# Optimization experiments

Hardware: AMD Instinct MI355X
Metric: run time of the kernel (lower is better)

## Reference

```python
import jax, jax.numpy as jnp
import numpy as np

B, H, W, DIM = 2, 128, 128, 256
HEADS, DHEAD = 16, 64
INNER = HEADS * DHEAD  # 1024
EPS = 1e-5  # BatchNorm eps


def _dwconv(x, w, groups):
    # x: [b, c_in, h, w], w: [c_out, c_in//groups, 3, 3], pad=1, stride=1
    return jax.lax.conv_general_dilated(
        x, w, window_strides=(1, 1), padding=((1, 1), (1, 1)),
        dimension_numbers=('NCHW', 'OIHW', 'NCHW'), feature_group_count=groups)


def _bn(x, gamma, beta, mean, var):
    # inference-mode BatchNorm2d over channel dim of NCHW
    inv = gamma * jax.lax.rsqrt(var + EPS)
    return (x - mean[None, :, None, None]) * inv[None, :, None, None] + beta[None, :, None, None]


def setup_inputs() -> dict:
    key = jax.random.key(0)
    ks = jax.random.split(key, 12)
    d = {}
    d['x_in'] = jax.random.normal(ks[0], (B, H, W, DIM), jnp.float32)
    def convw(k, cout):
        return jax.random.normal(k, (cout, 1, 3, 3), jnp.float32) * 0.1
    d['wq'] = convw(ks[1], INNER)
    d['wk'] = convw(ks[2], INNER)
    d['wv'] = convw(ks[3], INNER)
    for name, k in zip(('q', 'k', 'v'), (ks[4], ks[5], ks[6])):
        k0, k1 = jax.random.split(k)
        d[f'bn{name}_g'] = 1.0 + 0.1 * jax.random.normal(k0, (INNER,), jnp.float32)
        d[f'bn{name}_b'] = 0.05 * jax.random.normal(k1, (INNER,), jnp.float32)
        d[f'bn{name}_m'] = jnp.zeros((INNER,), jnp.float32)
        d[f'bn{name}_v'] = jnp.ones((INNER,), jnp.float32)
    d['rescale'] = jnp.ones((HEADS, 1, 1), jnp.float32)
    d['proj_w'] = jax.random.normal(ks[7], (DIM, INNER), jnp.float32) / np.sqrt(INNER).astype(np.float32)
    d['proj_b'] = jnp.zeros((DIM,), jnp.float32)
    d['pos_w1'] = convw(ks[8], DIM)
    d['pos_w2'] = convw(ks[9], DIM)
    return d


def _forward(x_in, wq, wk, wv,
             bnq_g, bnq_b, bnq_m, bnq_v,
             bnk_g, bnk_b, bnk_m, bnk_v,
             bnv_g, bnv_b, bnv_m, bnv_v,
             rescale, proj_w, proj_b, pos_w1, pos_w2):
    b, h, w, c = x_in.shape
    n = h * w
    x = jnp.transpose(x_in, (0, 3, 1, 2))  # [b, c, h, w]

    def proj_path(wc, g, be, m, va):
        y = _bn(_dwconv(x, wc, c), g, be, m, va)        # [b, INNER, h, w]
        return y.reshape(b, INNER, n).transpose(0, 2, 1)  # 'b c h w -> b (h w) c'

    q_inp = proj_path(wq, bnq_g, bnq_b, bnq_m, bnq_v)  # [b, n, INNER]
    k_inp = proj_path(wk, bnk_g, bnk_b, bnk_m, bnk_v)
    v_inp = proj_path(wv, bnv_g, bnv_b, bnv_m, bnv_v)

    def to_heads(t):
        # 'b n (h d) -> b h n d' then transpose(-2,-1) -> [b, heads, d, n]
        return t.reshape(b, n, HEADS, DHEAD).transpose(0, 2, 3, 1)

    q = to_heads(q_inp)
    k = to_heads(k_inp)
    v = to_heads(v_inp)
    # L2 normalize along token dim (last axis), torch F.normalize eps=1e-12
    q = q / jnp.clip(jnp.linalg.norm(q, axis=-1, keepdims=True), 1e-12)
    k = k / jnp.clip(jnp.linalg.norm(k, axis=-1, keepdims=True), 1e-12)

    attn = jnp.einsum('bhdn,bhen->bhde', k, q) * rescale[None]  # [b, heads, d, d]
    attn = jax.nn.softmax(attn, axis=-1)
    xo = jnp.einsum('bhde,bhen->bhdn', attn, v)  # [b, heads, d, n]
    # faithful to torch: raw reshape of [b, heads, d, n] -> [b, n, heads*d]
    xo = xo.reshape(b, n, HEADS * DHEAD)

    out_c = (xo @ proj_w.T + proj_b).reshape(b, h, w, c)

    vp = (v_inp @ proj_w.T + proj_b).reshape(b, h, w, c).transpose(0, 3, 1, 2)
    pe = _dwconv(jax.nn.gelu(_dwconv(vp, pos_w1, c), approximate=False), pos_w2, c)
    out_p = pe.transpose(0, 2, 3, 1)
    return out_c + out_p


def reference(x_in, wq, wk, wv,
              bnq_g, bnq_b, bnq_m, bnq_v,
              bnk_g, bnk_b, bnk_m, bnk_v,
              bnv_g, bnv_b, bnv_m, bnv_v,
              rescale, proj_w, proj_b, pos_w1, pos_w2):
    return _forward(x_in, wq, wk, wv,
                    bnq_g, bnq_b, bnq_m, bnq_v,
                    bnk_g, bnk_b, bnk_m, bnk_v,
                    bnv_g, bnv_b, bnv_m, bnv_v,
                    rescale, proj_w, proj_b, pos_w1, pos_w2)
```

## Files before the change

kernel.cpp:

```cpp
#include <hip/hip_runtime.h>

#define NTOK 16384
#define CDIM 256
#define INNER 1024
#define WW 128
#define HH 128

typedef unsigned short bf16_t;
typedef __bf16 bf16x8 __attribute__((ext_vector_type(8)));
typedef float f32x4 __attribute__((ext_vector_type(4)));

__device__ __forceinline__ float bf2f(bf16_t u) {
    union { unsigned int i; float f; } x;
    x.i = ((unsigned int)u) << 16;
    return x.f;
}
__device__ __forceinline__ bf16_t f2bf(float f) {
    union { float f; unsigned int i; } x;
    x.f = f;
    unsigned int r = x.i + 0x7FFFu + ((x.i >> 16) & 1u);
    return (bf16_t)(r >> 16);
}
__device__ __forceinline__ unsigned int cvtpk(float a, float b) {
    unsigned int r;
    asm("v_cvt_pk_bf16_f32 %0, %1, %2" : "=v"(r) : "v"(a), "v"(b));
    return r;
}

static const size_t OFF_VT   = 16777216;
static const size_t OFF_XO   = 83886080;
static const size_t OFF_VP   = 150994944;
static const size_t OFF_PE2  = 184549376;
static const size_t OFF_WBF  = 201326592;
static const size_t OFF_S    = 218103808;
static const size_t OFF_SSQ  = 218628096;
static const size_t OFF_SSK  = 218636288;

__global__ __launch_bounds__(512, 4) void k12_fused(
    const float* __restrict__ x,
    const float* __restrict__ wq, const float* __restrict__ wk, const float* __restrict__ wv,
    const float* __restrict__ qg, const float* __restrict__ qb, const float* __restrict__ qm, const float* __restrict__ qv,
    const float* __restrict__ kg, const float* __restrict__ kb, const float* __restrict__ km, const float* __restrict__ kv_,
    const float* __restrict__ vg, const float* __restrict__ vb, const float* __restrict__ vm, const float* __restrict__ vv,
    bf16_t* __restrict__ vt, float* __restrict__ S,
    float* __restrict__ ssq, float* __restrict__ ssk) {
    int chunk = blockIdx.x;
    int h = blockIdx.y;
    int b = blockIdx.z;
    int y0 = chunk * 8;

    __shared__ ushort taps[16][10][132];
    __shared__ ushort Qs[64][72];
    __shared__ ushort Ks[64][72];
    __shared__ unsigned int Vs32[64][34];

    int tid = threadIdx.x;
    int lane = tid & 63, wave = tid >> 6;

    {
        const float* xb = x + (size_t)b * NTOK * CDIM + h * 16;
        for (int u = tid; u < 5200; u += 512) {
            int pos = u >> 2, quad = u & 3;
            int i = pos / 130, c = pos - i * 130;
            int gy = y0 - 1 + i, gx = c - 1;
            if (gy >= 0 && gy < HH && gx >= 0 && gx < WW) {
                float4 v = *(const float4*)&xb[(size_t)(gy * WW + gx) * CDIM + quad * 4];
                taps[quad * 4 + 0][i][c] = f2bf(v.x);
                taps[quad * 4 + 1][i][c] = f2bf(v.y);
                taps[quad * 4 + 2][i][c] = f2bf(v.z);
                taps[quad * 4 + 3][i][c] = f2bf(v.w);
            } else {
                taps[quad * 4 + 0][i][c] = 0;
                taps[quad * 4 + 1][i][c] = 0;
                taps[quad * 4 + 2][i][c] = 0;
                taps[quad * 4 + 3][i][c] = 0;
            }
        }
    }

    int tq = tid & 15;
    int pc = (tid >> 4) & 15;
    int ts = tid >> 8;

    const float* wsrc = ts ? wk : wq;
    const float* gp = ts ? kg : qg;
    const float* bp = ts ? kb : qb;
    const float* mp = ts ? km : qm;
    const float* vp_ = ts ? kv_ : qv;
    int chbase = h * 64 + pc * 4;
    float wQK[4][9], shQK[4];
#pragma unroll
    for (int s = 0; s < 4; s++) {
        int ch = chbase + s;
        float sc = gp[ch] * rsqrtf(vp_[ch] + 1e-5f);
        shQK[s] = bp[ch] - mp[ch] * sc;
#pragma unroll
        for (int t = 0; t < 9; t++) wQK[s][t] = wsrc[(size_t)ch * 9 + t] * sc;
    }
    float wV[2][9], shV[2];
#pragma unroll
    for (int sv = 0; sv < 2; sv++) {
        int ch = chbase + 2 * ts + sv;
        float sc = vg[ch] * rsqrtf(vv[ch] + 1e-5f);
        shV[sv] = vb[ch] - vm[ch] * sc;
#pragma unroll
        for (int t = 0; t < 9; t++) wV[sv][t] = wv[(size_t)ch * 9 + t] * sc;
    }

    ushort (*QK)[72] = ts ? Ks : Qs;

    int wm = wave & 1;
    int wn4 = wave >> 1;
    int qd = lane >> 4, l16 = lane & 15;
    f32x4 acc[2];
    acc[0] = (f32x4){0.f, 0.f, 0.f, 0.f};
    acc[1] = (f32x4){0.f, 0.f, 0.f, 0.f};

    int vrow = tid >> 3;
    int vseg = tid & 7;
    bf16_t* vtb = vt + (size_t)b * 16777216 + (size_t)h * 64;

    float ssl[4] = {0.f, 0.f, 0.f, 0.f};

    __syncthreads();

#pragma unroll 1
    for (int kc = 0; kc < 1024; kc += 64) {
        int grp = kc >> 6;
        int ly = grp >> 1;
        int xh = (grp & 1) << 6;
        int x0 = xh + tq * 4;

        float tp[3][6];
#pragma unroll
        for (int i = 0; i < 3; i++) {
            const ushort* rp = &taps[pc][ly + i][x0];
            ushort4 u4 = *(const ushort4*)rp;
            ushort2 u2 = *(const ushort2*)(rp + 4);
            tp[i][0] = bf2f(u4.x); tp[i][1] = bf2f(u4.y);
            tp[i][2] = bf2f(u4.z); tp[i][3] = bf2f(u4.w);
            tp[i][4] = bf2f(u2.x); tp[i][5] = bf2f(u2.y);
        }

#pragma unroll
        for (int s = 0; s < 4; s++) {
            float o0 = shQK[s], o1 = shQK[s], o2 = shQK[s], o3 = shQK[s];
#pragma unroll
            for (int i = 0; i < 3; i++) {
                float wa = wQK[s][i * 3 + 0], wb = wQK[s][i * 3 + 1], wc = wQK[s][i * 3 + 2];
                o0 += wa * tp[i][0] + wb * tp[i][1] + wc * tp[i][2];
                o1 += wa * tp[i][1] + wb * tp[i][2] + wc * tp[i][3];
                o2 += wa * tp[i][2] + wb * tp[i][3] + wc * tp[i][4];
                o3 += wa * tp[i][3] + wb * tp[i][4] + wc * tp[i][5];
            }
            ssl[s] += o0 * o0 + o1 * o1 + o2 * o2 + o3 * o3;
            uint2 pk;
            pk.x = cvtpk(o0, o1);
            pk.y = cvtpk(o2, o3);
            *(uint2*)&QK[pc * 4 + s][tq * 4] = pk;
        }

        {
            float ov[2][4];
#pragma unroll
            for (int sv = 0; sv < 2; sv++) {
                float o0 = shV[sv], o1 = shV[sv], o2 = shV[sv], o3 = shV[sv];
#pragma unroll
                for (int i = 0; i < 3; i++) {
                    float wa = wV[sv][i * 3 + 0], wb = wV[sv][i * 3 + 1], wc = wV[sv][i * 3 + 2];
                    o0 += wa * tp[i][0] + wb * tp[i][1] + wc * tp[i][2];
                    o1 += wa * tp[i][1] + wb * tp[i][2] + wc * tp[i][3];
                    o2 += wa * tp[i][2] + wb * tp[i][3] + wc * tp[i][4];
                    o3 += wa * tp[i][3] + wb * tp[i][4] + wc * tp[i][5];
                }
                ov[sv][0] = o0; ov[sv][1] = o1; ov[sv][2] = o2; ov[sv][3] = o3;
            }
#pragma unroll
            for (int j = 0; j < 4; j++)
                Vs32[tq * 4 + j][pc * 2 + ts] = cvtpk(ov[0][j], ov[1][j]);
        }

        __syncthreads();

        {
            uint4 o4;
            o4.x = Vs32[vrow][vseg * 4 + 0];
            o4.y = Vs32[vrow][vseg * 4 + 1];
            o4.z = Vs32[vrow][vseg * 4 + 2];
            o4.w = Vs32[vrow][vseg * 4 + 3];
            *(uint4*)&vtb[(size_t)(chunk * 1024 + kc + vrow) * 1024 + vseg * 8] = o4;
        }

#pragma unroll
        for (int kk = 0; kk < 64; kk += 32) {
            bf16x8 af0 = *(const bf16x8*)&Ks[wm * 32 + l16][kk + qd * 8];
            bf16x8 af1 = *(const bf16x8*)&Ks[wm * 32 + 16 + l16][kk + qd * 8];
            bf16x8 bf0 = *(const bf16x8*)&Qs[wn4 * 16 + l16][kk + qd * 8];
            acc[0] = __builtin_amdgcn_mfma_f32_16x16x32_bf16(af0, bf0, acc[0], 0, 0, 0);
            acc[1] = __builtin_amdgcn_mfma_f32_16x16x32_bf16(af1, bf0, acc[1], 0, 0, 0);
        }

        __syncthreads();
    }

    float* Sb = S + (size_t)(b * 16 + h) * 4096;
#pragma unroll
    for (int i = 0; i < 2; i++)
#pragma unroll
        for (int r = 0; r < 4; r++) {
            int d = wm * 32 + i * 16 + qd * 4 + r;
            int e = wn4 * 16 + l16;
            atomicAdd(&Sb[(size_t)d * 64 + e], acc[i][r]);
        }

#pragma unroll
    for (int s = 0; s < 4; s++) {
        float v = ssl[s];
#pragma unroll
        for (int o = 1; o < 16; o <<= 1) v += __shfl_xor(v, o, 64);
        ssl[s] = v;
    }
    if ((lane & 15) == 0) {
        float* dst = (ts ? ssk : ssq) + b * INNER + chbase;
        atomicAdd(&dst[0], ssl[0]);
        atomicAdd(&dst[1], ssl[1]);
        atomicAdd(&dst[2], ssl[2]);
        atomicAdd(&dst[3], ssl[3]);
    }
}

__global__ __launch_bounds__(64) void k3_softmax(float* __restrict__ S,
                                                 const float* __restrict__ ssq,
                                                 const float* __restrict__ ssk,
                                                 const float* __restrict__ rescale) {
    int bh = blockIdx.x;
    int b = bh >> 4, h = bh & 15;
    int d = threadIdx.x;
    __shared__ float rq[64];
    int cbase = b * INNER + h * 64;
    rq[d] = 1.0f / fmaxf(sqrtf(ssq[cbase + d]), 1e-12f);
    float rk = 1.0f / fmaxf(sqrtf(ssk[cbase + d]), 1e-12f);
    __syncthreads();
    float rsc = rescale[h];
    const float* row = S + (size_t)bh * 4096 + (size_t)d * 64;
    float sv[64];
    float mx = -3.4e38f;
#pragma unroll
    for (int e = 0; e < 64; e++) {
        sv[e] = row[e] * rk * rq[e] * rsc;
        mx = fmaxf(mx, sv[e]);
    }
    float sum = 0.f;
#pragma unroll
    for (int e = 0; e < 64; e++) {
        sv[e] = expf(sv[e] - mx);
        sum += sv[e];
    }
    float inv = 1.0f / sum;
    __syncthreads();
    ushort* attn = (ushort*)((char*)S + (size_t)bh * 16384);
#pragma unroll
    for (int e = 0; e < 64; e++) attn[d * 64 + e] = f2bf(sv[e] * inv);
}

__global__ __launch_bounds__(256) void cvt_w(const float* __restrict__ w,
                                             bf16_t* __restrict__ wbf) {
    int i = (blockIdx.x * 256 + threadIdx.x) * 4;
    float4 f = *(const float4*)&w[i];
    ushort4 r;
    r.x = f2bf(f.x); r.y = f2bf(f.y); r.z = f2bf(f.z); r.w = f2bf(f.w);
    *(ushort4*)&wbf[i] = r;
}

__global__ __launch_bounds__(256) void k4_mfma(const float* __restrict__ Sbase,
                                               const bf16_t* __restrict__ vt,
                                               bf16_t* __restrict__ xo) {
    int tt = blockIdx.x;
    int h = blockIdx.y;
    int b = blockIdx.z;
    int bh = b * 16 + h;
    const ushort* attn = (const ushort*)((const char*)Sbase + (size_t)bh * 16384);
    __shared__ ushort As[64][72];
    __shared__ ushort Bs[128][72];
    int tid = threadIdx.x, lane = tid & 63, wave = tid >> 6;
    int wm = wave & 1, wn = wave >> 1;
    int qd = lane >> 4, l16 = lane & 15;
    int r0 = tid >> 3, c0 = (tid & 7) * 8;
#pragma unroll
    for (int l = 0; l < 2; l++) {
        int row = r0 + l * 32;
        *(uint4*)&As[row][c0] = *(const uint4*)&attn[row * 64 + c0];
    }
    const bf16_t* vtb = vt + (size_t)b * 16777216 + (size_t)(tt * 128) * 1024 + h * 64;
#pragma unroll
    for (int l = 0; l < 4; l++) {
        int row = r0 + l * 32;
        *(uint4*)&Bs[row][c0] = *(const uint4*)&vtb[(size_t)row * 1024 + c0];
    }
    __syncthreads();
    f32x4 acc[2][4];
#pragma unroll
    for (int i = 0; i < 2; i++)
#pragma unroll
        for (int j = 0; j < 4; j++) acc[i][j] = (f32x4){0.f, 0.f, 0.f, 0.f};
#pragma unroll
    for (int kk = 0; kk < 64; kk += 32) {
        bf16x8 af[2], bfr[4];
#pragma unroll
        for (int i = 0; i < 2; i++)
            af[i] = *(const bf16x8*)&As[wm * 32 + i * 16 + l16][kk + qd * 8];
#pragma unroll
        for (int j = 0; j < 4; j++)
            bfr[j] = *(const bf16x8*)&Bs[wn * 64 + j * 16 + l16][kk + qd * 8];
#pragma unroll
        for (int i = 0; i < 2; i++)
#pragma unroll
            for (int j = 0; j < 4; j++)
                acc[i][j] = __builtin_amdgcn_mfma_f32_16x16x32_bf16(af[i], bfr[j], acc[i][j], 0, 0, 0);
    }
    bf16_t* xob = xo + (size_t)b * 16777216 + (size_t)(h * 64) * NTOK + (size_t)tt * 128;
#pragma unroll
    for (int i = 0; i < 2; i++)
#pragma unroll
        for (int j = 0; j < 4; j++)
#pragma unroll
            for (int r = 0; r < 4; r++) {
                int d = wm * 32 + i * 16 + qd * 4 + r;
                int t = wn * 64 + j * 16 + l16;
                xob[(size_t)d * NTOK + t] = f2bf(acc[i][j][r]);
            }
}

template <int FUSE_PE2>
__global__ __launch_bounds__(256) void gemm_tn(
    const bf16_t* __restrict__ A, const bf16_t* __restrict__ B,
    const float* __restrict__ pb, void* __restrict__ Cv,
    int lda, int ldb, int ldc, int K,
    long strideA, long strideB, long strideC, int bias_on_n,
    const bf16_t* __restrict__ pe2) {
    int mb = blockIdx.x, nb = blockIdx.y, b = blockIdx.z;
    A += (size_t)b * strideA;
    B += (size_t)b * strideB;
    __shared__ ushort smem[2 * 128 * 72];
    ushort (*As)[72] = (ushort(*)[72])smem;
    ushort (*Bs)[72] = (ushort(*)[72])(smem + 128 * 72);
    int tid = threadIdx.x;
    int lane = tid & 63, wave = tid >> 6;
    int wm = wave & 1, wn = wave >> 1;
    int q = lane >> 4, l16 = lane & 15;
    f32x4 acc[4][4];
#pragma unroll
    for (int i = 0; i < 4; i++)
#pragma unroll
        for (int j = 0; j < 4; j++) acc[i][j] = (f32x4){0.f, 0.f, 0.f, 0.f};
    const bf16_t* Ab = A + (size_t)mb * 128 * lda;
    const bf16_t* Bb = B + (size_t)nb * 128 * ldb;
    int r0 = tid >> 3;
    int c0 = (tid & 7) * 8;
#pragma unroll 1
    for (int kc = 0; kc < K; kc += 64) {
#pragma unroll
        for (int l = 0; l < 4; l++) {
            int row = l * 32 + r0;
            *(uint4*)&As[row][c0] = *(const uint4*)&Ab[(size_t)row * lda + kc + c0];
            *(uint4*)&Bs[row][c0] = *(const uint4*)&Bb[(size_t)row * ldb + kc + c0];
        }
        __syncthreads();
#pragma unroll
        for (int kk = 0; kk < 64; kk += 32) {
            bf16x8 af[4], bfr[4];
#pragma unroll
            for (int i = 0; i < 4; i++)
                af[i] = *(const bf16x8*)&As[wm * 64 + i * 16 + l16][kk + q * 8];
#pragma unroll
            for (int j = 0; j < 4; j++)
                bfr[j] = *(const bf16x8*)&Bs[wn * 64 + j * 16 + l16][kk + q * 8];
#pragma unroll
            for (int i = 0; i < 4; i++)
#pragma unroll
                for (int j = 0; j < 4; j++)
                    acc[i][j] = __builtin_amdgcn_mfma_f32_16x16x32_bf16(af[i], bfr[j], acc[i][j], 0, 0, 0);
        }
        __syncthreads();
    }
    if (FUSE_PE2) {
        const bf16_t* peb = pe2 + (size_t)b * 4194304;
        int gm0 = mb * 128, gn0 = nb * 128;
        for (int u = tid; u < 128 * 16; u += 256) {
            int row = u >> 4, seg = u & 15;
            *(uint4*)&smem[row * 132 + seg * 8] =
                *(const uint4*)&peb[(size_t)(gn0 + row) * NTOK + gm0 + seg * 8];
        }
        __syncthreads();
        float* C = (float*)Cv + (size_t)b * strideC;
#pragma unroll
        for (int i = 0; i < 4; i++) {
#pragma unroll
            for (int j = 0; j < 4; j++) {
                int n = wn * 64 + j * 16 + l16;
                int gn = gn0 + n;
                int m0 = wm * 64 + i * 16 + q * 4;
                ushort4 pv4 = *(const ushort4*)&smem[n * 132 + m0];
                float bias = pb[gn];
#pragma unroll
                for (int r = 0; r < 4; r++) {
                    ushort pu = (r == 0) ? pv4.x : ((r == 1) ? pv4.y : ((r == 2) ? pv4.z : pv4.w));
                    C[(size_t)(gm0 + m0 + r) * ldc + gn] = acc[i][j][r] + bias + bf2f(pu);
                }
            }
        }
    } else {
        bf16_t* C = (bf16_t*)Cv + (size_t)b * strideC;
#pragma unroll
        for (int i = 0; i < 4; i++) {
#pragma unroll
            for (int j = 0; j < 4; j++) {
                int n = wn * 64 + j * 16 + l16;
                int gn = nb * 128 + n;
#pragma unroll
                for (int r = 0; r < 4; r++) {
                    int m = wm * 64 + i * 16 + q * 4 + r;
                    int gm = mb * 128 + m;
                    float bias = bias_on_n ? pb[gn] : pb[gm];
                    C[(size_t)gm * ldc + gn] = f2bf(acc[i][j][r] + bias);
                }
            }
        }
    }
}

__global__ __launch_bounds__(256) void k_pos_fused(const bf16_t* __restrict__ vp,
                                                   const float* __restrict__ w1t,
                                                   const float* __restrict__ w2t,
                                                   bf16_t* __restrict__ pe2) {
    int ychunk = blockIdx.x;
    int ch = blockIdx.y;
    int b = blockIdx.z;
    int y0 = ychunk * 8;
    __shared__ float t1[12][132];
    __shared__ float t2[10][132];
    const bf16_t* plane = vp + (size_t)b * 4194304 + (size_t)ch * NTOK;
    for (int idx = threadIdx.x; idx < 12 * 132; idx += 256) {
        int i = idx / 132, c = idx % 132;
        int gy = y0 - 2 + i, gx = c - 2;
        float val = 0.f;
        if (gy >= 0 && gy < HH && gx >= 0 && gx < WW) val = bf2f(plane[gy * WW + gx]);
        t1[i][c] = val;
    }
    float wa[9], wb[9];
#pragma unroll
    for (int t = 0; t < 9; t++) {
        wa[t] = w1t[(size_t)ch * 9 + t];
        wb[t] = w2t[(size_t)ch * 9 + t];
    }
    __syncthreads();
    for (int idx = threadIdx.x; idx < 10 * 130; idx += 256) {
        int i = idx / 130, c1 = idx % 130;
        int yy = y0 - 1 + i, xx = c1 - 1;
        float val = 0.f;
        if (yy >= 0 && yy < HH && xx >= 0 && xx < WW) {
            float a = wa[0] * t1[i][c1]     + wa[1] * t1[i][c1 + 1]     + wa[2] * t1[i][c1 + 2]
                    + wa[3] * t1[i + 1][c1] + wa[4] * t1[i + 1][c1 + 1] + wa[5] * t1[i + 1][c1 + 2]
                    + wa[6] * t1[i + 2][c1] + wa[7] * t1[i + 2][c1 + 1] + wa[8] * t1[i + 2][c1 + 2];
            val = 0.5f * a * (1.0f + erff(a * 0.70710678118654752f));
        }
        t2[i][c1] = val;
    }
    __syncthreads();
    int x = threadIdx.x & 127;
    int half = threadIdx.x >> 7;
    bf16_t* oplane = pe2 + (size_t)b * 4194304 + (size_t)ch * NTOK;
#pragma unroll
    for (int rp = 0; rp < 4; rp++) {
        int r = rp * 2 + half;
        float acc = wb[0] * t2[r][x]     + wb[1] * t2[r][x + 1]     + wb[2] * t2[r][x + 2]
                  + wb[3] * t2[r + 1][x] + wb[4] * t2[r + 1][x + 1] + wb[5] * t2[r + 1][x + 2]
                  + wb[6] * t2[r + 2][x] + wb[7] * t2[r + 2][x + 1] + wb[8] * t2[r + 2][x + 2];
        oplane[(size_t)(y0 + r) * WW + x] = f2bf(acc);
    }
}

extern "C" void kernel_launch(void* const* d_in, const int* in_sizes, int n_in,
                              void* d_out, int out_size, void* d_ws, size_t ws_size,
                              hipStream_t stream) {
    const float* x_in    = (const float*)d_in[0];
    const float* wq      = (const float*)d_in[1];
    const float* wk      = (const float*)d_in[2];
    const float* wv      = (const float*)d_in[3];
    const float* qg      = (const float*)d_in[4];
    const float* qb      = (const float*)d_in[5];
    const float* qm      = (const float*)d_in[6];
    const float* qv      = (const float*)d_in[7];
    const float* kg      = (const float*)d_in[8];
    const float* kb      = (const float*)d_in[9];
    const float* km      = (const float*)d_in[10];
    const float* kv_     = (const float*)d_in[11];
    const float* vg      = (const float*)d_in[12];
    const float* vb      = (const float*)d_in[13];
    const float* vm      = (const float*)d_in[14];
    const float* vv      = (const float*)d_in[15];
    const float* rescale = (const float*)d_in[16];
    const float* proj_w  = (const float*)d_in[17];
    const float* proj_b  = (const float*)d_in[18];
    const float* pos_w1  = (const float*)d_in[19];
    const float* pos_w2  = (const float*)d_in[20];

    char* ws = (char*)d_ws;
    bf16_t* vt   = (bf16_t*)(ws + OFF_VT);
    bf16_t* xo   = (bf16_t*)(ws + OFF_XO);
    bf16_t* vp   = (bf16_t*)(ws + OFF_VP);
    bf16_t* pe2  = (bf16_t*)(ws + OFF_PE2);
    bf16_t* wbf  = (bf16_t*)(ws + OFF_WBF);
    float* S     = (float*)(ws + OFF_S);
    float* ssq   = (float*)(ws + OFF_SSQ);
    float* ssk   = (float*)(ws + OFF_SSK);

    hipMemsetAsync(ws + OFF_S, 0, (size_t)540672, stream);

    k12_fused<<<dim3(16, 16, 2), 512, 0, stream>>>(x_in, wq, wk, wv,
                                                   qg, qb, qm, qv,
                                                   kg, kb, km, kv_,
                                                   vg, vb, vm, vv,
                                                   vt, S, ssq, ssk);
    k3_softmax<<<dim3(32), 64, 0, stream>>>(S, ssq, ssk, rescale);
    cvt_w<<<dim3(256), 256, 0, stream>>>(proj_w, wbf);
    k4_mfma<<<dim3(128, 16, 2), 256, 0, stream>>>(S, vt, xo);
    gemm_tn<0><<<dim3(2, 128, 2), 256, 0, stream>>>(wbf, vt, proj_b, vp,
                                                    1024, 1024, 16384, 1024,
                                                    0L, 16777216L, 4194304L, 0, nullptr);
    k_pos_fused<<<dim3(16, 256, 2), 256, 0, stream>>>(vp, pos_w1, pos_w2, pe2);
    gemm_tn<1><<<dim3(128, 2, 2), 256, 0, stream>>>(xo, wbf, proj_b, d_out,
                                                    1024, 1024, 256, 1024,
                                                    16777216L, 0L, 4194304L, 1, pe2);
}
```

Baseline: 318.2 us.

## Prefetch input tap rows into registers during loop, use lightweight barriers

Result: slower. 364.9 us (+14.7%).

```diff
diff --git a/kernel.cpp b/kernel.cpp
--- a/kernel.cpp
+++ b/kernel.cpp
@@ -56,25 +56,23 @@
 
     int tid = threadIdx.x;
     int lane = tid & 63, wave = tid >> 6;
-
-    {
-        const float* xb = x + (size_t)b * NTOK * CDIM + h * 16;
-        for (int u = tid; u < 5200; u += 512) {
-            int pos = u >> 2, quad = u & 3;
-            int i = pos / 130, c = pos - i * 130;
-            int gy = y0 - 1 + i, gx = c - 1;
-            if (gy >= 0 && gy < HH && gx >= 0 && gx < WW) {
-                float4 v = *(const float4*)&xb[(size_t)(gy * WW + gx) * CDIM + quad * 4];
-                taps[quad * 4 + 0][i][c] = f2bf(v.x);
-                taps[quad * 4 + 1][i][c] = f2bf(v.y);
-                taps[quad * 4 + 2][i][c] = f2bf(v.z);
-                taps[quad * 4 + 3][i][c] = f2bf(v.w);
-            } else {
-                taps[quad * 4 + 0][i][c] = 0;
-                taps[quad * 4 + 1][i][c] = 0;
-                taps[quad * 4 + 2][i][c] = 0;
-                taps[quad * 4 + 3][i][c] = 0;
-            }
+    const float* xb = x + (size_t)b * NTOK * CDIM + h * 16;
+
+    for (int u = tid; u < 1560; u += 512) {
+        int pos = u >> 2, quad = u & 3;
+        int i = pos / 130, c = pos - i * 130;
+        int gy = y0 - 1 + i, gx = c - 1;
+        if (gy >= 0 && gy < HH && gx >= 0 && gx < WW) {
+            float4 v = *(const float4*)&xb[(size_t)(gy * WW + gx) * CDIM + quad * 4];
+            taps[quad * 4 + 0][i][c] = f2bf(v.x);
+            taps[quad * 4 + 1][i][c] = f2bf(v.y);
+            taps[quad * 4 + 2][i][c] = f2bf(v.z);
+            taps[quad * 4 + 3][i][c] = f2bf(v.w);
+        } else {
+            taps[quad * 4 + 0][i][c] = 0;
+            taps[quad * 4 + 1][i][c] = 0;
+            taps[quad * 4 + 2][i][c] = 0;
+            taps[quad * 4 + 3][i][c] = 0;
         }
     }
 
@@ -120,6 +118,10 @@
     int vseg = tid & 7;
     bf16_t* vtb = vt + (size_t)b * 16777216 + (size_t)h * 64;
 
+    float4 pf0 = {0.f, 0.f, 0.f, 0.f};
+    float4 pf1 = {0.f, 0.f, 0.f, 0.f};
+    int pcc0 = tid >> 2, pq = tid & 3;
+
     float ssl[4] = {0.f, 0.f, 0.f, 0.f};
 
     __syncthreads();
@@ -130,6 +132,19 @@
         int ly = grp >> 1;
         int xh = (grp & 1) << 6;
         int x0 = xh + tq * 4;
+        int even = ((grp & 1) == 0);
+        int pr = ly + 3;
+
+        if (even && pr < 10) {
+            int gy = y0 - 1 + pr;
+            pf0 = (float4){0.f, 0.f, 0.f, 0.f};
+            pf1 = (float4){0.f, 0.f, 0.f, 0.f};
+            int gxa = pcc0 - 1;
+            if (gy < HH && gxa >= 0)
+                pf0 = *(const float4*)&xb[(size_t)(gy * WW + gxa) * CDIM + pq * 4];
+            if (tid < 4 && gy < HH)
+                pf1 = *(const float4*)&xb[(size_t)(gy * WW + 127) * CDIM + pq * 4];
+        }
 
         float tp[3][6];
 #pragma unroll
@@ -180,7 +195,22 @@
                 Vs32[tq * 4 + j][pc * 2 + ts] = cvtpk(ov[0][j], ov[1][j]);
         }
 
-        __syncthreads();
+        asm volatile("s_waitcnt lgkmcnt(0)" ::: "memory");
+        __builtin_amdgcn_s_barrier();
+
+        if (!even && pr < 10) {
+            taps[pq * 4 + 0][pr][pcc0] = f2bf(pf0.x);
+            taps[pq * 4 + 1][pr][pcc0] = f2bf(pf0.y);
+            taps[pq * 4 + 2][pr][pcc0] = f2bf(pf0.z);
+            taps[pq * 4 + 3][pr][pcc0] = f2bf(pf0.w);
+            if (tid < 8) {
+                int cc2 = 128 + (tid >> 2);
+                taps[pq * 4 + 0][pr][cc2] = f2bf(pf1.x);
+                taps[pq * 4 + 1][pr][cc2] = f2bf(pf1.y);
+                taps[pq * 4 + 2][pr][cc2] = f2bf(pf1.z);
+                taps[pq * 4 + 3][pr][cc2] = f2bf(pf1.w);
+            }
+        }
 
         {
             uint4 o4;
@@ -200,7 +230,8 @@
             acc[1] = __builtin_amdgcn_mfma_f32_16x16x32_bf16(af1, bf0, acc[1], 0, 0, 0);
         }
 
-        __syncthreads();
+        asm volatile("s_waitcnt lgkmcnt(0)" ::: "memory");
+        __builtin_amdgcn_s_barrier();
     }
 
     float* Sb = S + (size_t)(b * 16 + h) * 4096;
```
